# Kernel optimization log

Measured on AMD Instinct MI355X. Metric: run time of the kernel, lower is better.

## Reference

```python
import jax, jax.numpy as jnp
import numpy as np

MARGIN = 0.3
BIG = 1e5  # same constant the torch code uses to mask out same-id entries for the min


def setup_inputs() -> dict:
    key = jax.random.key(0)
    k1, k2, k3 = jax.random.split(key, 3)
    B, D, N_LUT, N_ID = 4096, 1024, 5000, 1024
    feat = jax.random.normal(k1, (B, D), dtype=jnp.float32)
    lut = jax.random.normal(k2, (N_LUT, D), dtype=jnp.float32)
    id = jax.random.randint(k3, (B,), 0, N_ID, dtype=jnp.int64)
    return {"feat": feat, "lut": lut, "id": id}


def reference(feat, lut, id):
    # feat_oim = lut[id]  (gather rows of the OIM lookup table)
    feat_oim = lut[id]  # (B, D)

    # Pairwise euclidean distance dist[i,j] = sqrt(||feat_i - feat_oim_j||^2 + 1e-12)
    # via the dot-product trick (avoids materializing the (B,B,D) diff tensor).
    sq_a = jnp.sum(feat * feat, axis=1)          # (B,)
    sq_b = jnp.sum(feat_oim * feat_oim, axis=1)  # (B,)
    sq = sq_a[:, None] + sq_b[None, :] - 2.0 * (feat @ feat_oim.T)  # (B, B)
    dist = jnp.sqrt(jnp.maximum(sq, 0.0) + 1e-12)

    # Masks (mode='id'):
    same_id = id[:, None] == id[None, :]               # (B, B) bool
    eye = jnp.eye(feat.shape[0], dtype=bool)
    positive_mask = same_id & ~eye

    # Batch-hard mining (n_dis=0):
    max_positive = jnp.max(dist * positive_mask.astype(dist.dtype), axis=1)   # hardest positive
    min_negative = jnp.min(dist + BIG * same_id.astype(dist.dtype), axis=1)   # hardest negative
    z = max_positive - min_negative

    # float margin path: hinge
    b_loss = jnp.maximum(z + MARGIN, 0.0)  # (B,)
    return b_loss
```

## Files before the change

kernel.cpp:

```cpp
#include <hip/hip_runtime.h>
#include <hip/hip_bf16.h>

#define B_N    4096
#define D_K    1024
#define N_C    1024
#define MARGIN 0.3f
#define BIGM   1e5f

typedef __attribute__((ext_vector_type(8))) short short8;
typedef __attribute__((ext_vector_type(4))) float f32x4;

__device__ inline ushort f2bf(float f) {
    unsigned u = __float_as_uint(f);
    unsigned r = (u + 0x7fffu + ((u >> 16) & 1u)) >> 16;
    return (ushort)r;
}

__device__ inline void async16(const ushort* g, ushort* l) {
    __builtin_amdgcn_global_load_lds(
        (const __attribute__((address_space(1))) void*)g,
        (__attribute__((address_space(3))) void*)l,
        16, 0, 0);
}

__global__ void prep_all(const float* __restrict__ feat,
                         const float* __restrict__ lut,
                         const int* __restrict__ id,
                         ushort* __restrict__ featB, ushort* __restrict__ lutB,
                         float* __restrict__ sq_a, float* __restrict__ sq_b,
                         int* __restrict__ cnt,
                         int* __restrict__ maxb, int* __restrict__ minb) {
    int b = blockIdx.x;
    int t = threadIdx.x;

    if (b == B_N + N_C) {
        __shared__ int hc[N_C];
        #pragma unroll
        for (int i = 0; i < 4; i++) hc[t * 4 + i] = 0;
        __syncthreads();
        #pragma unroll
        for (int i = 0; i < 16; i++) atomicAdd(&hc[id[t * 16 + i]], 1);
        __syncthreads();
        #pragma unroll
        for (int i = 0; i < 4; i++) cnt[t * 4 + i] = hc[t * 4 + i];
        return;
    }

    if (b < 16) {
        int i = b * 256 + t;
        maxb[i] = 0;
        minb[i] = 0x7F800000;
    }
    const float* src; ushort* dst; float* sq;
    if (b < B_N) {
        src = feat + (size_t)b * D_K;
        dst = featB + (size_t)b * D_K;
        sq  = sq_a + b;
    } else {
        int c = b - B_N;
        src = lut + (size_t)c * D_K;
        dst = lutB + (size_t)c * D_K;
        sq  = sq_b + c;
    }
    float4 v = ((const float4*)src)[t];
    float ss = v.x * v.x + v.y * v.y + v.z * v.z + v.w * v.w;
    ushort4 bb;
    bb.x = f2bf(v.x); bb.y = f2bf(v.y); bb.z = f2bf(v.z); bb.w = f2bf(v.w);
    ((ushort4*)dst)[t] = bb;

    int lane = t & 63, w = t >> 6;
    #pragma unroll
    for (int o = 1; o < 64; o <<= 1) ss += __shfl_xor(ss, o);
    __shared__ float red[4];
    if (lane == 0) red[w] = ss;
    __syncthreads();
    if (t == 0) *sq = red[0] + red[1] + red[2] + red[3];
}

__global__ __launch_bounds__(256, 4)
void dist_kernel(const ushort* __restrict__ A, const ushort* __restrict__ Bm,
                 const float* __restrict__ sqa, const float* __restrict__ sqb,
                 const int* __restrict__ ids, const int* __restrict__ cnt,
                 int* __restrict__ maxb, int* __restrict__ minb) {
    __shared__ ushort lds_[2 * 4096];

    const int t = threadIdx.x;
    const int lane = t & 63;
    const int wid = t >> 6;
    const int wr = wid >> 1;
    const int wc = wid & 1;
    const int l15 = lane & 15;
    const int h = lane >> 4;
    const int wo = wid * 512;

    const int bid = blockIdx.y * gridDim.x + blockIdx.x;
    const int swz = (bid & 7) * 128 + (bid >> 3);
    const int rb = swz >> 4, cb = swz & 15;

    int p = t * 8;
    int rp = p >> 6;
    int sl = ((p >> 3) & 7) ^ (rp & 7);
    int rr = rp * 2 + (sl >> 2);
    int jj = sl & 3;
    const ushort* gA = A  + (size_t)(rb * 64 + rr) * D_K + jj * 8;
    const ushort* gB = Bm + (size_t)(cb * 64 + rr) * D_K + jj * 8;

    const int par = (l15 & 1) << 2;
    int offA[2], offB[2];
    {
        int a0 = (wr * 32 + l15) >> 1;
        #pragma unroll
        for (int mf = 0; mf < 2; mf++) {
            int line = a0 + mf * 8;
            offA[mf] = line * 64 + (((par | h) ^ (line & 7)) << 3);
        }
        int b0 = (wc * 32 + l15) >> 1;
        #pragma unroll
        for (int nf = 0; nf < 2; nf++) {
            int line = b0 + nf * 8;
            offB[nf] = line * 64 + (((par | h) ^ (line & 7)) << 3);
        }
    }

    f32x4 acc[2][2] = {};

    async16(gA, lds_ + wo);
    async16(gB, lds_ + 2048 + wo);

    for (int kt = 0; kt < 32; ++kt) {
        const int s = kt & 1;
        const ushort* sA = lds_ + s * 4096;
        const ushort* sB = sA + 2048;

        if (kt < 31) {
            ushort* wb = lds_ + (s ^ 1) * 4096;
            async16(gA + (kt + 1) * 32, wb + wo);
            async16(gB + (kt + 1) * 32, wb + 2048 + wo);
            asm volatile("s_waitcnt vmcnt(2)" ::: "memory");
        } else {
            asm volatile("s_waitcnt vmcnt(0)" ::: "memory");
        }
        __builtin_amdgcn_sched_barrier(0);
        __builtin_amdgcn_s_barrier();
        __builtin_amdgcn_sched_barrier(0);

        short8 afv[2], bfv[2];
        #pragma unroll
        for (int mf = 0; mf < 2; mf++)
            afv[mf] = *(const short8*)(sA + offA[mf]);
        #pragma unroll
        for (int nf = 0; nf < 2; nf++)
            bfv[nf] = *(const short8*)(sB + offB[nf]);
        asm volatile("s_waitcnt lgkmcnt(0)" ::: "memory");
        __builtin_amdgcn_sched_barrier(0);
        __builtin_amdgcn_s_setprio(1);
        #pragma unroll
        for (int mf = 0; mf < 2; mf++)
            #pragma unroll
            for (int nf = 0; nf < 2; nf++)
                acc[mf][nf] = __builtin_amdgcn_mfma_f32_16x16x32_bf16(
                    afv[mf], bfv[nf], acc[mf][nf], 0, 0, 0);
        __builtin_amdgcn_s_setprio(0);
        __builtin_amdgcn_sched_barrier(0);
        __builtin_amdgcn_s_barrier();
    }

    int colg[2]; float sb2[2]; int c2[2];
    #pragma unroll
    for (int nf = 0; nf < 2; nf++) {
        int c = cb * 64 + wc * 32 + nf * 16 + l15;
        colg[nf] = c; sb2[nf] = sqb[c]; c2[nf] = cnt[c];
    }
    #pragma unroll
    for (int m = 0; m < 2; m++) {
        #pragma unroll
        for (int r = 0; r < 4; r++) {
            int row = rb * 64 + wr * 32 + m * 16 + h * 4 + r;
            float sa = sqa[row];
            int ida = ids[row];
            float mx = 0.0f, mn = 3.0e38f;
            #pragma unroll
            for (int nf = 0; nf < 2; nf++) {
                float s2 = sa + sb2[nf] - 2.0f * acc[m][nf][r];
                float d = sqrtf(fmaxf(s2, 0.0f) + 1e-12f);
                bool iseq = (colg[nf] == ida);
                float pv = (iseq && c2[nf] >= 2) ? d : 0.0f;
                float nv = (c2[nf] > 0 && !iseq) ? d : 3.0e38f;
                mx = fmaxf(mx, pv);
                mn = fminf(mn, nv);
            }
            #pragma unroll
            for (int o = 1; o < 16; o <<= 1) {
                mx = fmaxf(mx, __shfl_xor(mx, o));
                mn = fminf(mn, __shfl_xor(mn, o));
            }
            if (l15 == 0) {
                atomicMax(maxb + row, __float_as_int(mx));
                atomicMin(minb + row, __float_as_int(mn));
            }
        }
    }
}

__global__ void finalize_k(const int* __restrict__ maxb, const int* __restrict__ minb,
                           float* __restrict__ out) {
    int i = blockIdx.x * blockDim.x + threadIdx.x;
    if (i < B_N) {
        float z = __int_as_float(maxb[i]) - __int_as_float(minb[i]) + MARGIN;
        out[i] = fmaxf(z, 0.0f);
    }
}

extern "C" void kernel_launch(void* const* d_in, const int* in_sizes, int n_in,
                              void* d_out, int out_size, void* d_ws, size_t ws_size,
                              hipStream_t stream) {
    const float* feat = (const float*)d_in[0];
    const float* lut  = (const float*)d_in[1];
    const int*   id   = (const int*)d_in[2];
    float* out = (float*)d_out;

    char* ws = (char*)d_ws;
    ushort* featB = (ushort*)ws;
    ushort* lutB  = (ushort*)(ws + (size_t)B_N * D_K * 2);
    float*  sq_a  = (float*)(ws + (size_t)(B_N + N_C) * D_K * 2);
    float*  sq_b  = sq_a + B_N;
    int*    cnt   = (int*)(sq_b + N_C);
    int*    maxb  = cnt + N_C;
    int*    minb  = maxb + B_N;

    prep_all<<<B_N + N_C + 1, 256, 0, stream>>>(feat, lut, id, featB, lutB,
                                                sq_a, sq_b, cnt, maxb, minb);

    dim3 grid(N_C / 64, B_N / 64);
    dist_kernel<<<grid, 256, 0, stream>>>(featB, lutB, sq_a, sq_b, id, cnt,
                                          maxb, minb);

    finalize_k<<<16, 256, 0, stream>>>(maxb, minb, out);
}
```

Measured before the change: 39.46 us.

## Pre-pack feat into MFMA fragment layout and load A directly to registers with 128-row tiles

The prep kernel now writes the bf16 copy of feat in a fragment-packed layout, so each wave can load its A operands straight from global memory into registers with coalesced 16-byte loads, prefetched one k-step ahead. Only the lut tile still goes through LDS. Each block now covers 128 rows by 64 columns, with each wave owning 32 rows and all 64 columns, which halves the number of blocks and doubles the MFMA work per LDS read. This removes LDS traffic and staging for A and raises arithmetic intensity per block, at the cost of more registers per thread, fewer blocks in flight, and A data that is not shared between waves.

```diff
diff --git a/kernel.cpp b/kernel.cpp
--- a/kernel.cpp
+++ b/kernel.cpp
@@ -5,7 +5,6 @@
 #define D_K    1024
 #define N_C    1024
 #define MARGIN 0.3f
-#define BIGM   1e5f
 
 typedef __attribute__((ext_vector_type(8))) short short8;
 typedef __attribute__((ext_vector_type(4))) float f32x4;
@@ -26,7 +25,7 @@
 __global__ void prep_all(const float* __restrict__ feat,
                          const float* __restrict__ lut,
                          const int* __restrict__ id,
-                         ushort* __restrict__ featB, ushort* __restrict__ lutB,
+                         ushort* __restrict__ featP, ushort* __restrict__ lutB,
                          float* __restrict__ sq_a, float* __restrict__ sq_b,
                          int* __restrict__ cnt,
                          int* __restrict__ maxb, int* __restrict__ minb) {
@@ -51,22 +50,23 @@
         maxb[i] = 0;
         minb[i] = 0x7F800000;
     }
-    const float* src; ushort* dst; float* sq;
-    if (b < B_N) {
-        src = feat + (size_t)b * D_K;
-        dst = featB + (size_t)b * D_K;
-        sq  = sq_a + b;
-    } else {
-        int c = b - B_N;
-        src = lut + (size_t)c * D_K;
-        dst = lutB + (size_t)c * D_K;
-        sq  = sq_b + c;
-    }
+    const float* src; float* sq;
+    if (b < B_N) { src = feat + (size_t)b * D_K;          sq = sq_a + b; }
+    else         { src = lut + (size_t)(b - B_N) * D_K;   sq = sq_b + (b - B_N); }
+
     float4 v = ((const float4*)src)[t];
     float ss = v.x * v.x + v.y * v.y + v.z * v.z + v.w * v.w;
     ushort4 bb;
     bb.x = f2bf(v.x); bb.y = f2bf(v.y); bb.z = f2bf(v.z); bb.w = f2bf(v.w);
-    ((ushort4*)dst)[t] = bb;
+
+    if (b < B_N) {
+        int g = b >> 4, rl = b & 15;
+        int kt = t >> 3, h = (t >> 1) & 3, e0 = (t & 1) * 4;
+        size_t off = ((size_t)g * 32 + kt) * 512 + (rl + h * 16) * 8 + e0;
+        *(ushort4*)(featP + off) = bb;
+    } else {
+        ((ushort4*)(lutB + (size_t)(b - B_N) * D_K))[t] = bb;
+    }
 
     int lane = t & 63, w = t >> 6;
     #pragma unroll
@@ -78,23 +78,20 @@
 }
 
 __global__ __launch_bounds__(256, 4)
-void dist_kernel(const ushort* __restrict__ A, const ushort* __restrict__ Bm,
+void dist_kernel(const ushort* __restrict__ Ap, const ushort* __restrict__ Bm,
                  const float* __restrict__ sqa, const float* __restrict__ sqb,
                  const int* __restrict__ ids, const int* __restrict__ cnt,
                  int* __restrict__ maxb, int* __restrict__ minb) {
-    __shared__ ushort lds_[2 * 4096];
+    __shared__ __align__(16) ushort lB[2][2048];
 
     const int t = threadIdx.x;
     const int lane = t & 63;
     const int wid = t >> 6;
-    const int wr = wid >> 1;
-    const int wc = wid & 1;
     const int l15 = lane & 15;
     const int h = lane >> 4;
-    const int wo = wid * 512;
 
     const int bid = blockIdx.y * gridDim.x + blockIdx.x;
-    const int swz = (bid & 7) * 128 + (bid >> 3);
+    const int swz = (bid & 7) * 64 + (bid >> 3);
     const int rb = swz >> 4, cb = swz & 15;
 
     int p = t * 8;
@@ -102,85 +99,80 @@
     int sl = ((p >> 3) & 7) ^ (rp & 7);
     int rr = rp * 2 + (sl >> 2);
     int jj = sl & 3;
-    const ushort* gA = A  + (size_t)(rb * 64 + rr) * D_K + jj * 8;
     const ushort* gB = Bm + (size_t)(cb * 64 + rr) * D_K + jj * 8;
+    const int wo = wid * 512;
 
     const int par = (l15 & 1) << 2;
-    int offA[2], offB[2];
-    {
-        int a0 = (wr * 32 + l15) >> 1;
-        #pragma unroll
-        for (int mf = 0; mf < 2; mf++) {
-            int line = a0 + mf * 8;
-            offA[mf] = line * 64 + (((par | h) ^ (line & 7)) << 3);
-        }
-        int b0 = (wc * 32 + l15) >> 1;
-        #pragma unroll
-        for (int nf = 0; nf < 2; nf++) {
-            int line = b0 + nf * 8;
-            offB[nf] = line * 64 + (((par | h) ^ (line & 7)) << 3);
-        }
-    }
-
-    f32x4 acc[2][2] = {};
-
-    async16(gA, lds_ + wo);
-    async16(gB, lds_ + 2048 + wo);
-
-    for (int kt = 0; kt < 32; ++kt) {
-        const int s = kt & 1;
-        const ushort* sA = lds_ + s * 4096;
-        const ushort* sB = sA + 2048;
-
-        if (kt < 31) {
-            ushort* wb = lds_ + (s ^ 1) * 4096;
-            async16(gA + (kt + 1) * 32, wb + wo);
-            async16(gB + (kt + 1) * 32, wb + 2048 + wo);
-            asm volatile("s_waitcnt vmcnt(2)" ::: "memory");
-        } else {
-            asm volatile("s_waitcnt vmcnt(0)" ::: "memory");
-        }
-        __builtin_amdgcn_sched_barrier(0);
-        __builtin_amdgcn_s_barrier();
-        __builtin_amdgcn_sched_barrier(0);
-
-        short8 afv[2], bfv[2];
-        #pragma unroll
-        for (int mf = 0; mf < 2; mf++)
-            afv[mf] = *(const short8*)(sA + offA[mf]);
-        #pragma unroll
-        for (int nf = 0; nf < 2; nf++)
-            bfv[nf] = *(const short8*)(sB + offB[nf]);
-        asm volatile("s_waitcnt lgkmcnt(0)" ::: "memory");
-        __builtin_amdgcn_sched_barrier(0);
-        __builtin_amdgcn_s_setprio(1);
-        #pragma unroll
-        for (int mf = 0; mf < 2; mf++)
-            #pragma unroll
-            for (int nf = 0; nf < 2; nf++)
-                acc[mf][nf] = __builtin_amdgcn_mfma_f32_16x16x32_bf16(
-                    afv[mf], bfv[nf], acc[mf][nf], 0, 0, 0);
-        __builtin_amdgcn_s_setprio(0);
-        __builtin_amdgcn_sched_barrier(0);
-        __builtin_amdgcn_s_barrier();
-    }
-
-    int colg[2]; float sb2[2]; int c2[2];
-    #pragma unroll
-    for (int nf = 0; nf < 2; nf++) {
-        int c = cb * 64 + wc * 32 + nf * 16 + l15;
+    int offB[4];
+    #pragma unroll
+    for (int nf = 0; nf < 4; nf++) {
+        int line = (l15 >> 1) + nf * 8;
+        offB[nf] = line * 64 + (((par | h) ^ (line & 7)) << 3);
+    }
+
+    const ushort* pa0 = Ap + ((size_t)(rb * 8 + wid * 2 + 0) * 32) * 512 + lane * 8;
+    const ushort* pa1 = Ap + ((size_t)(rb * 8 + wid * 2 + 1) * 32) * 512 + lane * 8;
+
+    f32x4 acc[2][4] = {};
+    short8 aE0, aE1, aO0, aO1, bfv[4];
+
+    async16(gB, &lB[0][0] + wo);
+    aE0 = *(const short8*)(pa0);
+    aE1 = *(const short8*)(pa1);
+
+#define MFMA16(av0, av1)                                                    \
+    _Pragma("unroll") for (int nf = 0; nf < 4; nf++) {                      \
+        acc[0][nf] = __builtin_amdgcn_mfma_f32_16x16x32_bf16(               \
+            av0, bfv[nf], acc[0][nf], 0, 0, 0);                             \
+        acc[1][nf] = __builtin_amdgcn_mfma_f32_16x16x32_bf16(               \
+            av1, bfv[nf], acc[1][nf], 0, 0, 0);                             \
+    }
+
+#define ITER(KT, C0, C1, N0, N1)                                            \
+    {                                                                       \
+        const int s_ = (KT) & 1;                                            \
+        if ((KT) < 31) {                                                    \
+            async16(gB + ((KT) + 1) * 32, &lB[s_ ^ 1][0] + wo);             \
+            N0 = *(const short8*)(pa0 + ((KT) + 1) * 512);                  \
+            N1 = *(const short8*)(pa1 + ((KT) + 1) * 512);                  \
+            __builtin_amdgcn_sched_barrier(0);                              \
+            asm volatile("s_waitcnt vmcnt(5)" ::: "memory");                \
+        } else {                                                            \
+            asm volatile("s_waitcnt vmcnt(0)" ::: "memory");                \
+        }                                                                   \
+        __builtin_amdgcn_sched_barrier(0);                                  \
+        __builtin_amdgcn_s_barrier();               \
+        __builtin_amdgcn_sched_barrier(0);                                  \
+        _Pragma("unroll") for (int nf = 0; nf < 4; nf++)                    \
+            bfv[nf] = *(const short8*)(&lB[s_][0] + offB[nf]);              \
+        MFMA16(C0, C1);                                                     \
+        __builtin_amdgcn_sched_barrier(0);                                  \
+        __builtin_amdgcn_s_barrier();                \
+    }
+
+    for (int kt = 0; kt < 32; kt += 2) {
+        ITER(kt,     aE0, aE1, aO0, aO1);
+        ITER(kt + 1, aO0, aO1, aE0, aE1);
+    }
+#undef ITER
+#undef MFMA16
+
+    int colg[4]; float sb2[4]; int c2[4];
+    #pragma unroll
+    for (int nf = 0; nf < 4; nf++) {
+        int c = cb * 64 + nf * 16 + l15;
         colg[nf] = c; sb2[nf] = sqb[c]; c2[nf] = cnt[c];
     }
     #pragma unroll
     for (int m = 0; m < 2; m++) {
         #pragma unroll
         for (int r = 0; r < 4; r++) {
-            int row = rb * 64 + wr * 32 + m * 16 + h * 4 + r;
+            int row = rb * 128 + wid * 32 + m * 16 + h * 4 + r;
             float sa = sqa[row];
             int ida = ids[row];
             float mx = 0.0f, mn = 3.0e38f;
             #pragma unroll
-            for (int nf = 0; nf < 2; nf++) {
+            for (int nf = 0; nf < 4; nf++) {
                 float s2 = sa + sb2[nf] - 2.0f * acc[m][nf][r];
                 float d = sqrtf(fmaxf(s2, 0.0f) + 1e-12f);
                 bool iseq = (colg[nf] == ida);
@@ -220,7 +212,7 @@
     float* out = (float*)d_out;
 
     char* ws = (char*)d_ws;
-    ushort* featB = (ushort*)ws;
+    ushort* featP = (ushort*)ws;
     ushort* lutB  = (ushort*)(ws + (size_t)B_N * D_K * 2);
     float*  sq_a  = (float*)(ws + (size_t)(B_N + N_C) * D_K * 2);
     float*  sq_b  = sq_a + B_N;
@@ -228,11 +220,11 @@
     int*    maxb  = cnt + N_C;
     int*    minb  = maxb + B_N;
 
-    prep_all<<<B_N + N_C + 1, 256, 0, stream>>>(feat, lut, id, featB, lutB,
+    prep_all<<<B_N + N_C + 1, 256, 0, stream>>>(feat, lut, id, featP, lutB,
                                                 sq_a, sq_b, cnt, maxb, minb);
 
-    dim3 grid(N_C / 64, B_N / 64);
-    dist_kernel<<<grid, 256, 0, stream>>>(featB, lutB, sq_a, sq_b, id, cnt,
+    dim3 grid(N_C / 64, B_N / 128);
+    dist_kernel<<<grid, 256, 0, stream>>>(featP, lutB, sq_a, sq_b, id, cnt,
                                           maxb, minb);
 
     finalize_k<<<16, 256, 0, stream>>>(maxb, minb, out);
```

Result: no change. 38.81 us (-1.6%).
